# Kernel optimization log

Measured on AMD Instinct MI355X. Metric: run time of the kernel, lower is better.

## Reference

```python
import jax, jax.numpy as jnp
from jax import lax
import numpy as np

# Dims matching init_kwargs / input_specs
B, R, C, CIN, COUT, W, CT = 8, 96, 64, 8, 64, 8, 4


def setup_inputs() -> dict:
    key = jax.random.key(0)
    ks = jax.random.split(key, 16)
    s = 0.05
    n = lambda k, shp: s * jax.random.normal(k, shp, jnp.float32)
    return {
        "x": jax.random.normal(ks[0], (B, R, C, CIN, 1), jnp.float32),
        "x_mark": jax.random.normal(ks[1], (B, R, C, CIN, CT), jnp.float32),
        # hidden_MLP_data: Conv1d(c_in -> c_in*c_out, k=W, groups=c_in) -> per-group in=1
        "Wd": n(ks[2], (CIN * COUT, 1, W)),
        "bd": n(ks[3], (CIN * COUT,)),
        # hidden_MLP_mark: Conv1d(c_in*CT -> c_in*c_out, k=W, groups=c_in) -> per-group in=CT
        "Wm": n(ks[4], (CIN * COUT, CT, W)),
        "bm": n(ks[5], (CIN * COUT,)),
        # gate_data: k=1 grouped conv, per-group 1 -> 2*c_out; stored einsum-friendly [g, 2*c_out]
        "Gd": n(ks[6], (CIN, 2 * COUT)),
        "bgd": n(ks[7], (CIN, 2 * COUT)),
        # gate_mark: per-group CT -> 2*c_out
        "Gm": n(ks[8], (CIN, 2 * COUT, CT)),
        "bgm": n(ks[9], (CIN, 2 * COUT)),
        # gate_hid: per-group c_out -> 2*c_out
        "Gh": n(ks[10], (CIN, 2 * COUT, COUT)),
        "bgh": n(ks[11], (CIN, 2 * COUT)),
        # fc: Conv1d(c_in*c_out -> c_in*c_out, k=seq_R, groups=c_in) -> [g, o, i, R]
        "Fw": n(ks[12], (CIN, COUT, COUT, R)),
        "bf": n(ks[13], (CIN, COUT)),
    }


def _grouped_conv1d(xa, w, b, groups):
    # xa: [N, Cin, L], w: [Cout, Cin//groups, K]
    y = lax.conv_general_dilated(
        xa, w, window_strides=(1,), padding="VALID",
        dimension_numbers=("NCH", "OIH", "NCH"), feature_group_count=groups)
    return y + b[None, :, None]


def reference(x, x_mark, Wd, bd, Wm, bm, Gd, bgd, Gm, bgm, Gh, bgh, Fw, bf):
    Bv, Rv, Cv, cin, _ = x.shape
    ct = x_mark.shape[-1]
    cout = Gh.shape[-1]
    Wk = Wd.shape[-1]

    # ---- deal(): causal windowed grouped conv over R ----
    # pad W zeros in front along R, drop last step -> length R+W-1, VALID conv k=W -> R
    xz = jnp.concatenate([jnp.zeros((Bv, Wk, Cv, cin, 1), x.dtype), x], axis=1)
    xa = xz.transpose(0, 2, 3, 4, 1).reshape(Bv * Cv, cin, Rv + Wk)[:, :, :-1]
    Hd = _grouped_conv1d(xa, Wd, bd, cin)  # [B*C, cin*cout, R]

    mz = jnp.concatenate([jnp.zeros((Bv, Wk, Cv, cin, ct), x.dtype), x_mark], axis=1)
    ma = mz.transpose(0, 2, 3, 4, 1).reshape(Bv * Cv, cin * ct, Rv + Wk)[:, :, :-1]
    Hm = _grouped_conv1d(ma, Wm, bm, cin)

    hid = (Hd + Hm).reshape(Bv, Cv, cin, cout, Rv).transpose(0, 4, 1, 2, 3)  # [B,R,C,cin,cout]

    # ---- gated_unit(): kernel-1 grouped convs == per-group matmuls ----
    xs = x[..., 0]  # [B,R,C,cin]
    g = jnp.einsum("brcg,go->brcgo", xs, Gd) + bgd
    g = g + jnp.einsum("brcgt,got->brcgo", x_mark, Gm) + bgm
    g = g + jnp.einsum("brcgi,goi->brcgo", hid, Gh) + bgh
    sg = jax.nn.sigmoid(g[..., :cout])
    tg = jnp.tanh(g[..., cout:])
    hid = hid * sg + (1.0 - sg) * tg  # [B,R,C,cin,cout]

    # ---- fc: grouped conv with kernel==R -> full contraction over (in-chan, R) ----
    out = jnp.einsum("brcgi,goir->bcgo", hid, Fw) + bf  # [B,C,cin,cout]
    return out
```

## Files before the change

kernel.cpp:

```cpp
#include <hip/hip_runtime.h>
#include <hip/hip_bf16.h>
#include <math.h>

namespace {

typedef __attribute__((ext_vector_type(8))) short bh8;
typedef __attribute__((ext_vector_type(4))) short sh4;
typedef __attribute__((ext_vector_type(4))) float fx4;

constexpr int Rn = 96, Cn = 64, CINn = 8, COUTn = 64;
constexpr int NPOS = 8 * 96 * 64 * 8;
constexpr int PPG  = 8 * 96 * 64;
constexpr float NLOG2E = -1.4426950408889634f;
constexpr float LOG2E2 =  2.8853900817779268f;
constexpr size_t FEAT_OFF = 0;
constexpr size_t FWT_OFF  = (size_t)NPOS * 16;
constexpr size_t CA_OFF   = FWT_OFF + (size_t)NPOS * 16;
constexpr size_t GWT_OFF  = CA_OFF + 65536;

__device__ inline ushort f2b(float f) {
  __hip_bfloat16 h = __float2bfloat16(f);
  return __builtin_bit_cast(ushort, h);
}
__device__ inline unsigned cvtpk(float lo, float hi) {
  unsigned r;
  asm("v_cvt_pk_bf16_f32 %0, %1, %2" : "=v"(r) : "v"(lo), "v"(hi));
  return r;
}
__device__ inline int swz8(int bc, int rr, int ib) {
  return (bc * 1024 + rr * 128 + ib) ^ (((rr + bc) & 7) << 4);
}
__device__ inline int fswz(int l, int bc) {
  return (l * 16 + (bc ^ (l & 7))) * 8;
}

#define MFMA16(a, b, c) __builtin_amdgcn_mfma_f32_16x16x32_bf16((a), (b), (c), 0, 0, 0)

__global__ __launch_bounds__(512)
void prep_k(const float* __restrict__ x, const float* __restrict__ xm,
            const float* __restrict__ Fw, const float* __restrict__ Gh,
            const float* __restrict__ Gd, const float* __restrict__ bgd,
            const float* __restrict__ Gm, const float* __restrict__ bgm,
            const float* __restrict__ bgh,
            const float* __restrict__ Wd, const float* __restrict__ bd,
            const float* __restrict__ Wm, const float* __restrict__ bm,
            ushort* __restrict__ feat, ushort* __restrict__ FwT,
            ushort* __restrict__ GWT, ushort* __restrict__ cA,
            float* __restrict__ out)
{
  __shared__ float tile[64 * 97];
  const int bid = blockIdx.x, t = threadIdx.x;
  if (bid < 768) {
    const int pos = bid * 512 + t;
    const float xs = x[pos];
    const fx4 m = *(const fx4*)(xm + (size_t)pos * 4);
    bh8 o;
    o[0] = (short)f2b(xs);
    o[1] = (short)f2b(m[0]); o[2] = (short)f2b(m[1]);
    o[3] = (short)f2b(m[2]); o[4] = (short)f2b(m[3]);
    o[5] = (short)0x3F80; o[6] = 0; o[7] = 0;
    const int g = pos & 7, pb = pos >> 3;
    *(bh8*)(feat + ((size_t)g * PPG + pb) * 8) = o;
  } else if (bid < 1280) {
    const int go = bid - 768;
    const float* src = Fw + (size_t)go * 6144;
    ushort* dst = FwT + (size_t)go * 6144;
#pragma unroll
    for (int it = 0; it < 12; ++it) {
      const int idx = t + it * 512;
      tile[(idx / 96) * 97 + (idx % 96)] = src[idx];
    }
    __syncthreads();
#pragma unroll
    for (int it = 0; it < 12; ++it) {
      const int idx = t + it * 512;
      const int r = idx >> 6, i = idx & 63;
      dst[idx] = f2b(tile[i * 97 + r]);
    }
  } else if (bid < 1344) {
    const int e = (bid - 1280) * 512 + t;
    const int j = e & 7, lp = (e >> 3) & 63, sub = (e >> 9) & 7, g = e >> 12;
    const int il = lp >> 4, mr = lp & 15;
    const int o2 = (sub >> 2) * 64 + (sub & 3) * 16 + mr;
    float v = 0.f;
    if (il == 0) {
      if (j == 0)      v = Gd[g * 128 + o2];
      else if (j <= 4) v = Gm[(size_t)(g * 128 + o2) * 4 + (j - 1)];
      else if (j == 5) v = bgd[g * 128 + o2] + bgm[g * 128 + o2] + bgh[g * 128 + o2];
    }
    v *= (sub >= 4) ? LOG2E2 : NLOG2E;
    GWT[((size_t)(g * 24 + sub * 3 + 2) * 64 + lp) * 8 + j] = f2b(v);
  } else if (bid < 1408) {
    const int e = (bid - 1344) * 512 + t;
    const int g = e >> 12, co = (e >> 6) & 63, k = e & 63;
    const int tap = k >> 3, tch = k & 7;
    float v = 0.f;
    if (tch == 0)      v = Wd[(g * 64 + co) * 8 + tap];
    else if (tch <= 4) v = Wm[((g * 64 + co) * 4 + (tch - 1)) * 8 + tap];
    else if (tch == 5 && tap == 0) v = bd[g * 64 + co] + bm[g * 64 + co];
    cA[e] = f2b(v);
  } else if (bid < 1536) {
    const int e = (bid - 1408) * 512 + t;
    const int row = e >> 6, k = e & 63;
    const int g = row >> 7, o2 = row & 127;
    const int tap = k >> 3, tch = k & 7;
    const float* pA; int sA = 0; float mA = 0.f, mB = 0.f;
    const float* pB;
    if (tch == 0)      { pA = Wd + (size_t)(g * 64) * 8 + tap; sA = 8;  mA = 1.f; }
    else if (tch <= 4) { pA = Wm + ((size_t)(g * 64) * 4 + (tch - 1)) * 8 + tap; sA = 32; mA = 1.f; }
    else if (tch == 5 && tap == 0) { pA = bd + g * 64; sA = 1; mA = 1.f; mB = 1.f; }
    else               { pA = Wd; }
    pB = (mB != 0.f) ? (bm + g * 64) : pA;
    const float* gh = Gh + (size_t)(g * 128 + o2) * 64;
    float acc = 0.f;
#pragma unroll 8
    for (int i = 0; i < 64; ++i) {
      const float wv = fmaf(mB, pB[i], mA * pA[i * sA]);
      acc = fmaf(gh[i], wv, acc);
    }
    acc *= (o2 >= 64) ? LOG2E2 : NLOG2E;
    const int half = o2 >> 6, s = (o2 >> 4) & 3, mr = o2 & 15;
    const int sub = half * 4 + s, fs = k >> 5, lp = ((k & 31) >> 3) * 16 + mr, j = k & 7;
    GWT[((size_t)(g * 24 + sub * 3 + fs) * 64 + lp) * 8 + j] = f2b(acc);
  } else {
    out[(bid - 1536) * 512 + t] = 0.f;
  }
}

__global__ __launch_bounds__(512, 2)
void fused_v15(const ushort* __restrict__ feat, const ushort* __restrict__ FwT,
               const ushort* __restrict__ cA, const ushort* __restrict__ GWT,
               const float* __restrict__ bf, float* __restrict__ out)
{
  __shared__ __align__(16) ushort sTab[16384];
  __shared__ __align__(16) char sGat[2][16384];
  __shared__ __align__(16) ushort sFeat[2][2048];
  __shared__ float sRed[1024];

  const int t    = threadIdx.x;
  const int lane = t & 63;
  const int w    = t >> 6;
  const int il   = lane >> 4;
  const int mr   = lane & 15;
  const int bid  = blockIdx.x;
  const int g    = bid & 7;
  const int bcT  = (bid >> 3) & 31;
  const int chh  = bid >> 8;
  const ushort* fg = feat + (size_t)g * PPG * 8;
  const int s4   = w & 3, hf = w >> 2;
  const int tb   = lane * 8;

  const int pglob = w * 16 + mr;
  const int cbcl = pglob >> 3, crr = pglob & 7;

  const int sl = t >> 4, sbc = t & 15;
  const int sbcg = bcT * 16 + sbc;
  const size_t sprow = (size_t)((sbcg >> 6) * 96) * 64 + (sbcg & 63);
  const int sadr = fswz(sl, sbc);
  const bh8 zpad = {0, 0, 0, 0, 0, (short)0x3F80, 0, 0};

  *(bh8*)&sTab[w * 512 + tb] =
      *(const bh8*)(cA + g * 4096 + ((w >> 1) * 16 + mr) * 64 + (w & 1) * 32 + il * 8);
  {
    const ushort* gsrc = GWT + (size_t)g * 12288;
#pragma unroll
    for (int it = 0; it < 3; ++it) {
      const int idx = it * 512 + t;
      *(bh8*)&sTab[4096 + idx * 8] = *(const bh8*)(gsrc + idx * 8);
    }
  }
  if (t < 256) {
    const int q = chh * 48 - 8 + sl;
    *(bh8*)&sFeat[0][sadr] =
        (q >= 0) ? *(const bh8*)(fg + (sprow + (size_t)q * 64) * 8) : zpad;
  }

  const int a_b0 = fswz(crr + il, cbcl);
  const int a_b1 = fswz(crr + il + 4, cbcl);
  const int a_bx = fswz(crr + 8, cbcl);
  int wadr[4];
#pragma unroll
  for (int s = 0; s < 4; ++s) wadr[s] = swz8(cbcl, crr, s * 32 + il * 8);
  const ushort* fb0 = FwT + ((size_t)(g * 64 + s4 * 16 + mr) * 96) * 64 + 32 * hf + 8 * il;

  fx4 facc = {0.f, 0.f, 0.f, 0.f};
  __syncthreads();

  int cur = 0;
#pragma unroll 1
  for (int k6 = 0; k6 < 6; ++k6) {
    const int r0 = chh * 48 + k6 * 8;

    bh8 stg;
    const bool do_stage = (t < 256) && (k6 < 5);
    if (do_stage)
      stg = *(const bh8*)(fg + (sprow + (size_t)(r0 + sl) * 64) * 8);
    bh8 aF[8];
    {
      const ushort* fb = fb0 + (size_t)r0 * 64;
#pragma unroll
      for (int f = 0; f < 8; ++f) aF[f] = *(const bh8*)(fb + f * 64);
    }

    const bh8 b0 = *(const bh8*)&sFeat[cur][a_b0];
    const bh8 b1 = *(const bh8*)&sFeat[cur][a_b1];
    const bh8 bx = *(const bh8*)&sFeat[cur][a_bx];

    fx4 ah[4];
#pragma unroll
    for (int s = 0; s < 4; ++s) {
      const bh8 a0 = *(const bh8*)&sTab[(s * 2 + 0) * 512 + tb];
      const bh8 a1 = *(const bh8*)&sTab[(s * 2 + 1) * 512 + tb];
      fx4 a = {0.f, 0.f, 0.f, 0.f};
      a = MFMA16(a0, b0, a);
      a = MFMA16(a1, b1, a);
      ah[s] = a;
    }

    char* gbuf = sGat[k6 & 1];
#pragma unroll
    for (int s = 0; s < 4; ++s) {
      const int bs = (8 + s * 3) * 512 + tb;
      const int bt = (8 + (4 + s) * 3) * 512 + tb;
      fx4 aS = {0.f,0.f,0.f,0.f}, aT = {0.f,0.f,0.f,0.f};
      aS = MFMA16(*(const bh8*)&sTab[bs],        b0, aS);
      aS = MFMA16(*(const bh8*)&sTab[bs + 512],  b1, aS);
      aS = MFMA16(*(const bh8*)&sTab[bs + 1024], bx, aS);
      aT = MFMA16(*(const bh8*)&sTab[bt],        b0, aT);
      aT = MFMA16(*(const bh8*)&sTab[bt + 512],  b1, aT);
      aT = MFMA16(*(const bh8*)&sTab[bt + 1024], bx, aT);
      float hv[4];
#pragma unroll
      for (int cc = 0; cc < 4; ++cc) {
        const float sig = __builtin_amdgcn_rcpf(1.f + __builtin_amdgcn_exp2f(aS[cc]));
        const float th  = fmaf(-2.f, __builtin_amdgcn_rcpf(1.f + __builtin_amdgcn_exp2f(aT[cc])), 1.f);
        hv[cc] = fmaf(sig, ah[s][cc] - th, th);
      }
      uint2 pk;
      pk.x = cvtpk(hv[0], hv[1]);
      pk.y = cvtpk(hv[2], hv[3]);
      *(uint2*)(gbuf + wadr[s]) = pk;
    }

    if (do_stage) *(bh8*)&sFeat[cur ^ 1][sadr] = stg;
    __syncthreads();

#pragma unroll
    for (int f = 0; f < 8; ++f) {
      const bh8 bF = *(const bh8*)(gbuf + swz8(mr, f, 64 * hf + 16 * il));
      facc = MFMA16(aF[f], bF, facc);
    }
    cur ^= 1;
  }

  if (hf == 1) {
#pragma unroll
    for (int cc = 0; cc < 4; ++cc)
      sRed[s4 * 256 + (4 * il + cc) * 16 + mr] = facc[cc];
  }
  __syncthreads();
  if (hf == 0) {
    float* po = out + ((size_t)(bcT * 16 + mr) * 8 + g) * 64 + s4 * 16;
#pragma unroll
    for (int cc = 0; cc < 4; ++cc) {
      const int ol = 4 * il + cc;
      float v = facc[cc] + sRed[s4 * 256 + ol * 16 + mr];
      if (chh == 0) v += bf[g * 64 + s4 * 16 + ol];
      atomicAdd(po + ol, v);
    }
  }
}

}

extern "C" void kernel_launch(void* const* d_in, const int* in_sizes, int n_in,
                              void* d_out, int out_size, void* d_ws, size_t ws_size,
                              hipStream_t stream) {
  const float* x   = (const float*)d_in[0];
  const float* xm  = (const float*)d_in[1];
  const float* Wd  = (const float*)d_in[2];
  const float* bd  = (const float*)d_in[3];
  const float* Wm  = (const float*)d_in[4];
  const float* bm  = (const float*)d_in[5];
  const float* Gd  = (const float*)d_in[6];
  const float* bgd = (const float*)d_in[7];
  const float* Gm  = (const float*)d_in[8];
  const float* bgm = (const float*)d_in[9];
  const float* Gh  = (const float*)d_in[10];
  const float* bgh = (const float*)d_in[11];
  const float* Fw  = (const float*)d_in[12];
  const float* bf  = (const float*)d_in[13];
  float* outp = (float*)d_out;

  ushort* feat = (ushort*)((char*)d_ws + FEAT_OFF);
  ushort* FwT  = (ushort*)((char*)d_ws + FWT_OFF);
  ushort* cA   = (ushort*)((char*)d_ws + CA_OFF);
  ushort* GWT  = (ushort*)((char*)d_ws + GWT_OFF);

  prep_k<<<dim3(2048), dim3(512), 0, stream>>>(
      x, xm, Fw, Gh, Gd, bgd, Gm, bgm, bgh, Wd, bd, Wm, bm, feat, FwT, GWT, cA, outp);
  fused_v15<<<dim3(512), dim3(512), 0, stream>>>(feat, FwT, cA, GWT, bf, outp);
}
```

Before: 52.11 us.

## Software-pipeline fc MFMA one chunk behind gate compute and fuse gate math

Moves the fc contraction for chunk k-1 into iteration k, running it between the hidden MFMAs and the gate MFMAs so fc work overlaps with gate compute and only one barrier per iteration remains on the critical path. A tail block handles the last chunk. It also precomputes the swizzled LDS addresses and merges the sigmoid/tanh blend into one reciprocal of a product of exponentials. The risks are higher register pressure from holding the previous chunk's Fw fragments, and possible overflow or precision loss in the merged exponential form.

```diff
diff --git a/kernel.cpp b/kernel.cpp
--- a/kernel.cpp
+++ b/kernel.cpp
@@ -128,7 +128,7 @@
 }
 
 __global__ __launch_bounds__(512, 2)
-void fused_v15(const ushort* __restrict__ feat, const ushort* __restrict__ FwT,
+void fused_v16(const ushort* __restrict__ feat, const ushort* __restrict__ FwT,
                const ushort* __restrict__ cA, const ushort* __restrict__ GWT,
                const float* __restrict__ bf, float* __restrict__ out)
 {
@@ -182,6 +182,9 @@
 #pragma unroll
   for (int s = 0; s < 4; ++s) wadr[s] = swz8(cbcl, crr, s * 32 + il * 8);
   const ushort* fb0 = FwT + ((size_t)(g * 64 + s4 * 16 + mr) * 96) * 64 + 32 * hf + 8 * il;
+  int fadr[8];
+#pragma unroll
+  for (int f = 0; f < 8; ++f) fadr[f] = swz8(mr, f, 64 * hf + 16 * il);
 
   fx4 facc = {0.f, 0.f, 0.f, 0.f};
   __syncthreads();
@@ -195,11 +198,11 @@
     const bool do_stage = (t < 256) && (k6 < 5);
     if (do_stage)
       stg = *(const bh8*)(fg + (sprow + (size_t)(r0 + sl) * 64) * 8);
-    bh8 aF[8];
-    {
-      const ushort* fb = fb0 + (size_t)r0 * 64;
-#pragma unroll
-      for (int f = 0; f < 8; ++f) aF[f] = *(const bh8*)(fb + f * 64);
+    bh8 aFp[8];
+    if (k6 > 0) {
+      const ushort* fb = fb0 + (size_t)(r0 - 8) * 64;
+#pragma unroll
+      for (int f = 0; f < 8; ++f) aFp[f] = *(const bh8*)(fb + f * 64);
     }
 
     const bh8 b0 = *(const bh8*)&sFeat[cur][a_b0];
@@ -215,6 +218,15 @@
       a = MFMA16(a0, b0, a);
       a = MFMA16(a1, b1, a);
       ah[s] = a;
+    }
+
+    if (k6 > 0) {
+      const char* pbuf = sGat[(k6 - 1) & 1];
+#pragma unroll
+      for (int f = 0; f < 8; ++f) {
+        const bh8 bF = *(const bh8*)(pbuf + fadr[f]);
+        facc = MFMA16(aFp[f], bF, facc);
+      }
     }
 
     char* gbuf = sGat[k6 & 1];
@@ -232,9 +244,11 @@
       float hv[4];
 #pragma unroll
       for (int cc = 0; cc < 4; ++cc) {
-        const float sig = __builtin_amdgcn_rcpf(1.f + __builtin_amdgcn_exp2f(aS[cc]));
-        const float th  = fmaf(-2.f, __builtin_amdgcn_rcpf(1.f + __builtin_amdgcn_exp2f(aT[cc])), 1.f);
-        hv[cc] = fmaf(sig, ah[s][cc] - th, th);
+        const float E1 = __builtin_amdgcn_exp2f(aS[cc]);
+        const float E2 = __builtin_amdgcn_exp2f(aT[cc]);
+        const float bb = 1.f + E2;
+        const float num = fmaf(ah[s][cc], bb, fmaf(E1, E2, -E1));
+        hv[cc] = num * __builtin_amdgcn_rcpf((1.f + E1) * bb);
       }
       uint2 pk;
       pk.x = cvtpk(hv[0], hv[1]);
@@ -244,13 +258,18 @@
 
     if (do_stage) *(bh8*)&sFeat[cur ^ 1][sadr] = stg;
     __syncthreads();
-
+    cur ^= 1;
+  }
+
+  {
+    const ushort* fb = fb0 + (size_t)(chh * 48 + 40) * 64;
+    const char* pbuf = sGat[1];
 #pragma unroll
     for (int f = 0; f < 8; ++f) {
-      const bh8 bF = *(const bh8*)(gbuf + swz8(mr, f, 64 * hf + 16 * il));
-      facc = MFMA16(aF[f], bF, facc);
-    }
-    cur ^= 1;
+      const bh8 aFt = *(const bh8*)(fb + f * 64);
+      const bh8 bF = *(const bh8*)(pbuf + fadr[f]);
+      facc = MFMA16(aFt, bF, facc);
+    }
   }
 
   if (hf == 1) {
@@ -299,5 +318,5 @@
 
   prep_k<<<dim3(2048), dim3(512), 0, stream>>>(
       x, xm, Fw, Gh, Gd, bgd, Gm, bgm, bgh, Wd, bd, Wm, bm, feat, FwT, GWT, cA, outp);
-  fused_v15<<<dim3(512), dim3(512), 0, stream>>>(feat, FwT, cA, GWT, bf, outp);
-}
+  fused_v16<<<dim3(512), dim3(512), 0, stream>>>(feat, FwT, cA, GWT, bf, outp);
+}
```

Measured after the change: 54.82 us. 5.2% more time.
